# Kernel optimization log

Measured on AMD Instinct MI355X. Metric: run time of the kernel, lower is better.

Reference implementation:

```python
import jax, jax.numpy as jnp
import numpy as np

B, T, N, H, E, LH, OUT, D = 64, 12, 325, 64, 32, 128, 12, 1
META_OFF = 65  # x[..., :1] is the signal, x[..., 65:] is the 32-dim temporal meta input


def _mlp(meta, W1, b1, W2, b2):
    # meta: (B,E); W1: (4,E,LH); W2: (4,LH,O) -> (4,B,O); 4 = gates g,i,f,o
    h = jax.nn.relu(jnp.einsum('be,geh->gbh', meta, W1) + b1[:, None, :])
    return jnp.einsum('gbh,gho->gbo', h, W2) + b2[:, None, :]


def setup_inputs() -> dict:
    key = jax.random.key(0)
    ks = jax.random.split(key, 16)
    s = lambda k, shape: jax.random.normal(k, shape, dtype=jnp.float32) * 0.05
    return {
        'x': jax.random.normal(ks[0], (B, T, N, 1 + 64 + E), dtype=jnp.float32),
        'lwx_W1': s(ks[1], (4, E, LH)), 'lwx_b1': s(ks[2], (4, LH)),
        'lwx_W2': s(ks[3], (4, LH, D * H)), 'lwx_b2': s(ks[4], (4, D * H)),
        'lwh_W1': s(ks[5], (4, E, LH)), 'lwh_b1': s(ks[6], (4, LH)),
        'lwh_W2': s(ks[7], (4, LH, H * H)), 'lwh_b2': s(ks[8], (4, H * H)),
        'lb_W1': s(ks[9], (4, E, LH)), 'lb_b1': s(ks[10], (4, LH)),
        'lb_W2': s(ks[11], (4, LH, H)), 'lb_b2': s(ks[12], (4, H)),
        'fc1_W': s(ks[13], (H, H // 2)), 'fc1_b': jnp.zeros((H // 2,), jnp.float32),
        'fc2_W': s(ks[14], (H // 2, OUT * D)), 'fc2_b': jnp.zeros((OUT * D,), jnp.float32),
    }


def reference(x, lwx_W1, lwx_b1, lwx_W2, lwx_b2,
              lwh_W1, lwh_b1, lwh_W2, lwh_b2,
              lb_W1, lb_b1, lb_W2, lb_b2,
              fc1_W, fc1_b, fc2_W, fc2_b):
    batch = x.shape[0]
    meta = jnp.mean(x[:, :, 0, META_OFF:], axis=1)  # (B,E)
    xs = jnp.transpose(x[..., :D], (1, 0, 2, 3))    # (T,B,N,D)

    Wx = _mlp(meta, lwx_W1, lwx_b1, lwx_W2, lwx_b2).reshape(4, batch, D, H)
    Wh = _mlp(meta, lwh_W1, lwh_b1, lwh_W2, lwh_b2).reshape(4, batch, H, H)
    b = _mlp(meta, lb_W1, lb_b1, lb_W2, lb_b2).reshape(4, batch, 1, H)

    def step(carry, xt):
        h, c = carry
        # (4,B,N,H): per-batch weights -> batched matmuls for all 4 gates
        z = (jnp.einsum('bnd,gbdh->gbnh', xt, Wx)
             + jnp.einsum('bnh,gbhk->gbnk', h, Wh) + b)
        g = jnp.tanh(z[0])
        i = jax.nn.sigmoid(z[1])
        f = jax.nn.sigmoid(z[2])
        o = jax.nn.sigmoid(z[3])
        c = g * i + c * f
        h = jnp.tanh(c) * o
        return (h, c), None

    # h0=c0=0 reproduces the torch t==0 special case exactly
    h0 = jnp.zeros((batch, N, H), x.dtype)
    (h, _), _ = jax.lax.scan(step, (h0, h0), xs)

    out = jax.nn.relu(h)
    out = jax.nn.relu(out @ fc1_W + fc1_b) @ fc2_W + fc2_b  # (B,N,OUT*D)
    out = out.reshape(batch, N, OUT, D)
    return jnp.transpose(out, (0, 2, 1, 3))  # (B,OUT,N,D)
```

## Files before the change

kernel.cpp:

```cpp
#include <hip/hip_runtime.h>
#include <stdint.h>

#define TT 12
#define NN 325
#define HH 64
#define EE 32
#define LHH 128
#define OO 12
#define CIN 97
#define MOFF 65
#define BB 64

typedef __attribute__((ext_vector_type(8))) short bf8;
typedef __attribute__((ext_vector_type(4))) float f4;
typedef __attribute__((ext_vector_type(2))) float f2;

__device__ __forceinline__ float sigf(float x) {
  return __builtin_amdgcn_rcpf(1.f + __builtin_amdgcn_exp2f(-1.4426950408889634f * x));
}
__device__ __forceinline__ float tanhfast(float x) {
  return 1.f - 2.f * __builtin_amdgcn_rcpf(1.f + __builtin_amdgcn_exp2f(2.8853900817779268f * x));
}
__device__ __forceinline__ unsigned short f2bf(float f) {
  unsigned int u = __float_as_uint(f);
  u += 0x7fffu + ((u >> 16) & 1u);
  return (unsigned short)(u >> 16);
}
__device__ __forceinline__ float bf2f(unsigned short s) {
  return __uint_as_float(((unsigned int)s) << 16);
}

__global__ __launch_bounds__(256) void k_prep(
    const float* __restrict__ x,
    const float* __restrict__ xw1, const float* __restrict__ xb1,
    const float* __restrict__ xw2, const float* __restrict__ xb2,
    const float* __restrict__ hw1, const float* __restrict__ hb1,
    const float* __restrict__ hw2, const float* __restrict__ hb2,
    const float* __restrict__ bw1, const float* __restrict__ bb1,
    const float* __restrict__ bw2, const float* __restrict__ bb2,
    unsigned short* __restrict__ whb,
    float* __restrict__ wx_ws, float* __restrict__ bg_ws)
{
  const int bi = blockIdx.x, tid = threadIdx.x;
  const bool gemm = (bi < 1024);
  const int g  = gemm ? (bi >> 8) : ((bi - 1024) >> 2);
  const int bq = gemm ? (bi & 3) : ((bi - 1024) & 3);

  __shared__ float meta_s[16][EE];
  __shared__ float hbuf[2][16][132];

  for (int p = tid; p < 512; p += 256) {
    const int bl = p >> 5, e = p & 31;
    const int b = bq * 16 + bl;
    float s = 0.f;
    #pragma unroll
    for (int t = 0; t < TT; ++t)
      s += x[(size_t)((b * TT + t) * NN) * CIN + MOFF + e];
    meta_s[bl][e] = s * (1.f / 12.f);
  }
  __syncthreads();

  if (gemm) {
    const int i = (bi >> 2) & 63;
    for (int m = tid; m < 16 * LHH; m += 256) {
      const int bl = m >> 7, l = m & 127;
      float a = hb1[g * LHH + l];
      const float* w = hw1 + (size_t)g * (EE * LHH) + l;
      #pragma unroll
      for (int e = 0; e < EE; ++e) a = fmaf(meta_s[bl][e], w[e * LHH], a);
      hbuf[0][bl][l] = fmaxf(a, 0.f);
    }
    __syncthreads();

    const int r0 = (tid >> 5) * 2, j0 = (tid & 31) * 2;
    const float* w2p = hw2 + (size_t)(g * LHH) * 4096 + i * 64 + j0;
    float acc[2][2] = {};
    for (int l = 0; l < LHH; l += 4) {
      const f4 h0 = *(const f4*)&hbuf[0][r0][l];
      const f4 h1 = *(const f4*)&hbuf[0][r0 + 1][l];
      #pragma unroll
      for (int ll = 0; ll < 4; ++ll) {
        const f2 wv = *(const f2*)(w2p + (size_t)(l + ll) * 4096);
        acc[0][0] = fmaf(h0[ll], wv[0], acc[0][0]);
        acc[0][1] = fmaf(h0[ll], wv[1], acc[0][1]);
        acc[1][0] = fmaf(h1[ll], wv[0], acc[1][0]);
        acc[1][1] = fmaf(h1[ll], wv[1], acc[1][1]);
      }
    }

    const int kh = i >> 5, quad = (i >> 3) & 3, j8 = i & 7;
    #pragma unroll
    for (int rr = 0; rr < 2; ++rr) {
      const int b = bq * 16 + r0 + rr;
      #pragma unroll
      for (int jj = 0; jj < 2; ++jj) {
        const int j = j0 + jj;
        const float v = acc[rr][jj] + hb2[g * 4096 + i * 64 + j];
        const int col = g * 64 + j;
        const int nt = col >> 4, c16 = col & 15;
        const int lane = quad * 16 + c16;
        whb[(size_t)((b * 32 + kh * 16 + nt) * 64 + lane) * 8 + j8] = f2bf(v);
      }
    }
  } else {
    for (int m = tid; m < 2 * 16 * LHH; m += 256) {
      const int mlp = m >> 11, rem = m & 2047, bl = rem >> 7, l = rem & 127;
      const float* W1 = mlp ? bw1 : xw1;
      const float* B1 = mlp ? bb1 : xb1;
      float a = B1[g * LHH + l];
      const float* w = W1 + (size_t)g * (EE * LHH) + l;
      #pragma unroll
      for (int e = 0; e < EE; ++e) a = fmaf(meta_s[bl][e], w[e * LHH], a);
      hbuf[mlp][bl][l] = fmaxf(a, 0.f);
    }
    __syncthreads();

    const int h = tid & 63, bl0 = (tid >> 6) * 4;
    const float* wxp = xw2 + (size_t)g * (LHH * HH) + h;
    const float* wbp = bw2 + (size_t)g * (LHH * HH) + h;
    float accx[4], accb[4];
    #pragma unroll
    for (int k = 0; k < 4; ++k) {
      accx[k] = xb2[g * HH + h];
      accb[k] = bb2[g * HH + h];
    }
    for (int l = 0; l < LHH; ++l) {
      const float wxl = wxp[l * HH], wbl = wbp[l * HH];
      #pragma unroll
      for (int k = 0; k < 4; ++k) {
        accx[k] = fmaf(hbuf[0][bl0 + k][l], wxl, accx[k]);
        accb[k] = fmaf(hbuf[1][bl0 + k][l], wbl, accb[k]);
      }
    }
    #pragma unroll
    for (int k = 0; k < 4; ++k) {
      const int b = bq * 16 + bl0 + k;
      wx_ws[b * 256 + g * 64 + h] = accx[k];
      bg_ws[b * 256 + g * 64 + h] = accb[k];
    }
  }
}

__global__ __launch_bounds__(256, 3) void k_lstm(
    const float* __restrict__ x, const float* __restrict__ wx_ws,
    const float* __restrict__ bg_ws, const unsigned short* __restrict__ whb,
    const float* __restrict__ fc1W, const float* __restrict__ fc1b,
    const float* __restrict__ fc2W, const float* __restrict__ fc2b,
    float* __restrict__ out)
{
  const int rb = blockIdx.x, b = blockIdx.y, tid = threadIdx.x;
  const int wave = tid >> 6, lane = tid & 63, quad = lane >> 4, c16 = lane & 15;
  const int n0 = rb * 32;

  __shared__ __align__(16) unsigned short Hs[2][2][16][72];
  __shared__ float Xs[TT][32];
  __shared__ float fc1s[HH * 32];
  __shared__ float fc2s[32 * OO];
  __shared__ float HIDs[32][36];
  __shared__ float fc1bs[32];
  __shared__ float fc2bs[OO];

  for (int idx = tid; idx < TT * 32; idx += 256) {
    const int t = idx >> 5, r = idx & 31, n = n0 + r;
    Xs[t][r] = (n < NN) ? x[(size_t)((b * TT + t) * NN + n) * CIN] : 0.f;
  }
  for (int idx = tid; idx < HH * 32; idx += 256) fc1s[idx] = fc1W[idx];
  for (int idx = tid; idx < 32 * OO; idx += 256) fc2s[idx] = fc2W[idx];
  if (tid < 32) fc1bs[tid] = fc1b[tid];
  if (tid < OO) fc2bs[tid] = fc2b[tid];

  float wxv[4], bgv[4];
  #pragma unroll
  for (int g = 0; g < 4; ++g) {
    wxv[g] = wx_ws[b * 256 + g * 64 + wave * 16 + c16];
    bgv[g] = bg_ws[b * 256 + g * 64 + wave * 16 + c16];
  }
  bf8 wf[2][4];
  #pragma unroll
  for (int kh = 0; kh < 2; ++kh)
    #pragma unroll
    for (int g = 0; g < 4; ++g)
      wf[kh][g] = *(const bf8*)(whb + (size_t)((b * 32 + kh * 16 + g * 4 + wave) * 64 + lane) * 8);

  float cst[2][4];
  #pragma unroll
  for (int ta = 0; ta < 2; ++ta)
    #pragma unroll
    for (int r = 0; r < 4; ++r) cst[ta][r] = 0.f;

  __syncthreads();

  #pragma unroll 1
  for (int t = 0; t < TT; ++t) {
    bf8 af[2][2];
    if (t > 0) {
      #pragma unroll
      for (int ta = 0; ta < 2; ++ta) {
        af[ta][0] = *(const bf8*)&Hs[(t - 1) & 1][ta][c16][quad * 8];
        af[ta][1] = *(const bf8*)&Hs[(t - 1) & 1][ta][c16][32 + quad * 8];
      }
    }
    f4 ac[2][4];
    #pragma unroll
    for (int ta = 0; ta < 2; ++ta) {
      float xr[4];
      #pragma unroll
      for (int r = 0; r < 4; ++r) xr[r] = Xs[t][ta * 16 + quad * 4 + r];
      #pragma unroll
      for (int g = 0; g < 4; ++g)
        #pragma unroll
        for (int r = 0; r < 4; ++r)
          ac[ta][g][r] = fmaf(xr[r], wxv[g], bgv[g]);
    }
    if (t > 0) {
      #pragma unroll
      for (int ta = 0; ta < 2; ++ta)
        #pragma unroll
        for (int g = 0; g < 4; ++g) {
          ac[ta][g] = __builtin_amdgcn_mfma_f32_16x16x32_bf16(af[ta][0], wf[0][g], ac[ta][g], 0, 0, 0);
          ac[ta][g] = __builtin_amdgcn_mfma_f32_16x16x32_bf16(af[ta][1], wf[1][g], ac[ta][g], 0, 0, 0);
        }
    }
    #pragma unroll
    for (int ta = 0; ta < 2; ++ta)
      #pragma unroll
      for (int r = 0; r < 4; ++r) {
        const float gg = tanhfast(ac[ta][0][r]);
        const float ii = sigf(ac[ta][1][r]);
        const float ff = sigf(ac[ta][2][r]);
        const float oo = sigf(ac[ta][3][r]);
        const float cc = fmaf(gg, ii, cst[ta][r] * ff);
        cst[ta][r] = cc;
        const float hh = tanhfast(cc) * oo;
        Hs[t & 1][ta][quad * 4 + r][wave * 16 + c16] = f2bf(hh);
      }
    __syncthreads();
  }

  {
    const int row32 = tid & 31, uu = tid >> 5;
    const int ta = row32 >> 4, row = row32 & 15;
    float hacc[4];
    #pragma unroll
    for (int j = 0; j < 4; ++j) hacc[j] = fc1bs[uu * 4 + j];
    #pragma unroll
    for (int kc = 0; kc < 8; ++kc) {
      const bf8 hv = *(const bf8*)&Hs[1][ta][row][kc * 8];
      #pragma unroll
      for (int j8 = 0; j8 < 8; ++j8) {
        const float hk = fmaxf(bf2f((unsigned short)hv[j8]), 0.f);
        const int k = kc * 8 + j8;
        #pragma unroll
        for (int j = 0; j < 4; ++j)
          hacc[j] = fmaf(hk, fc1s[k * 32 + uu * 4 + j], hacc[j]);
      }
    }
    #pragma unroll
    for (int j = 0; j < 4; ++j)
      HIDs[row32][uu * 4 + j] = fmaxf(hacc[j], 0.f);
  }
  __syncthreads();
  for (int idx = tid; idx < 32 * OO; idx += 256) {
    const int o = idx >> 5, row32 = idx & 31;
    float a = fc2bs[o];
    #pragma unroll
    for (int k = 0; k < 32; ++k)
      a = fmaf(HIDs[row32][k], fc2s[k * OO + o], a);
    const int n = n0 + row32;
    if (n < NN)
      out[b * (OO * NN) + o * NN + n] = a;
  }
}

extern "C" void kernel_launch(void* const* d_in, const int* in_sizes, int n_in,
                              void* d_out, int out_size, void* d_ws, size_t ws_size,
                              hipStream_t stream) {
  const float* x    = (const float*)d_in[0];
  const float* xw1  = (const float*)d_in[1];
  const float* xb1  = (const float*)d_in[2];
  const float* xw2  = (const float*)d_in[3];
  const float* xb2  = (const float*)d_in[4];
  const float* hw1  = (const float*)d_in[5];
  const float* hb1  = (const float*)d_in[6];
  const float* hw2  = (const float*)d_in[7];
  const float* hb2  = (const float*)d_in[8];
  const float* bw1  = (const float*)d_in[9];
  const float* bb1  = (const float*)d_in[10];
  const float* bw2  = (const float*)d_in[11];
  const float* bb2  = (const float*)d_in[12];
  const float* fc1W = (const float*)d_in[13];
  const float* fc1b = (const float*)d_in[14];
  const float* fc2W = (const float*)d_in[15];
  const float* fc2b = (const float*)d_in[16];
  float* out = (float*)d_out;

  float* ws = (float*)d_ws;
  float* wx_ws = ws;
  float* bg_ws = ws + 16384;
  unsigned short* whb = (unsigned short*)(ws + 32768);

  k_prep<<<1040, 256, 0, stream>>>(x, xw1, xb1, xw2, xb2, hw1, hb1, hw2, hb2,
                                   bw1, bb1, bw2, bb2, whb, wx_ws, bg_ws);
  k_lstm<<<dim3(11, 64), 256, 0, stream>>>(x, wx_ws, bg_ws, whb,
                                           fc1W, fc1b, fc2W, fc2b, out);
}
```

Measured before the change: 236.7 us.

## Split meta mean into own kernel, stage W2 in LDS, pre-gather signal

Computes the temporal meta mean once per batch in a new small kernel, so the 1040 prep blocks no longer each re-read strided x. In the main prep kernel, the hw2 weight tile is first loaded cooperatively into shared memory in two halves, with coalesced reads, and the GEMM then reads from there. The gemm blocks also gather the signal channel of x into a compact buffer, so the LSTM kernel reads contiguous data instead of a stride of 97 floats. This adds one kernel launch and extra barriers, and raises the shared-memory footprint under a launch bound of 4 blocks.

Measured after the change: 232.1 us. -2.0%, faster.

```diff
diff --git a/kernel.cpp b/kernel.cpp
--- a/kernel.cpp
+++ b/kernel.cpp
@@ -30,15 +30,33 @@
   return __uint_as_float(((unsigned int)s) << 16);
 }
 
-__global__ __launch_bounds__(256) void k_prep(
-    const float* __restrict__ x,
+__global__ __launch_bounds__(256) void k_meta0(
+    const float* __restrict__ x, float* __restrict__ meta_ws)
+{
+  const int b = blockIdx.x, tid = threadIdx.x;
+  __shared__ float mpart[TT][EE];
+  for (int idx = tid; idx < TT * EE; idx += 256) {
+    const int t = idx >> 5, e = idx & 31;
+    mpart[t][e] = x[(size_t)((b * TT + t) * NN) * CIN + MOFF + e];
+  }
+  __syncthreads();
+  if (tid < EE) {
+    float s = 0.f;
+    #pragma unroll
+    for (int t = 0; t < TT; ++t) s += mpart[t][tid];
+    meta_ws[b * EE + tid] = s * (1.f / 12.f);
+  }
+}
+
+__global__ __launch_bounds__(256, 4) void k_main(
+    const float* __restrict__ x, const float* __restrict__ meta_ws,
     const float* __restrict__ xw1, const float* __restrict__ xb1,
     const float* __restrict__ xw2, const float* __restrict__ xb2,
     const float* __restrict__ hw1, const float* __restrict__ hb1,
     const float* __restrict__ hw2, const float* __restrict__ hb2,
     const float* __restrict__ bw1, const float* __restrict__ bb1,
     const float* __restrict__ bw2, const float* __restrict__ bb2,
-    unsigned short* __restrict__ whb,
+    unsigned short* __restrict__ whb, float* __restrict__ xg,
     float* __restrict__ wx_ws, float* __restrict__ bg_ws)
 {
   const int bi = blockIdx.x, tid = threadIdx.x;
@@ -48,20 +66,26 @@
 
   __shared__ float meta_s[16][EE];
   __shared__ float hbuf[2][16][132];
-
-  for (int p = tid; p < 512; p += 256) {
-    const int bl = p >> 5, e = p & 31;
-    const int b = bq * 16 + bl;
-    float s = 0.f;
-    #pragma unroll
-    for (int t = 0; t < TT; ++t)
-      s += x[(size_t)((b * TT + t) * NN) * CIN + MOFF + e];
-    meta_s[bl][e] = s * (1.f / 12.f);
-  }
+  __shared__ float w2s[64][64];
+
+  for (int p = tid; p < 16 * EE; p += 256)
+    meta_s[p >> 5][p & 31] = meta_ws[(bq * 16 + (p >> 5)) * EE + (p & 31)];
   __syncthreads();
 
   if (gemm) {
     const int i = (bi >> 2) & 63;
+
+    {
+      const int flat = bi * 244 + tid;
+      if (tid < 244 && flat < BB * TT * NN) {
+        const int b = flat / (TT * NN);
+        const int r = flat - b * (TT * NN);
+        const int t = r / NN;
+        const int n = r - t * NN;
+        xg[flat] = x[(size_t)((b * TT + t) * NN + n) * CIN];
+      }
+    }
+
     for (int m = tid; m < 16 * LHH; m += 256) {
       const int bl = m >> 7, l = m & 127;
       float a = hb1[g * LHH + l];
@@ -70,21 +94,27 @@
       for (int e = 0; e < EE; ++e) a = fmaf(meta_s[bl][e], w[e * LHH], a);
       hbuf[0][bl][l] = fmaxf(a, 0.f);
     }
-    __syncthreads();
 
     const int r0 = (tid >> 5) * 2, j0 = (tid & 31) * 2;
-    const float* w2p = hw2 + (size_t)(g * LHH) * 4096 + i * 64 + j0;
     float acc[2][2] = {};
-    for (int l = 0; l < LHH; l += 4) {
-      const f4 h0 = *(const f4*)&hbuf[0][r0][l];
-      const f4 h1 = *(const f4*)&hbuf[0][r0 + 1][l];
-      #pragma unroll
-      for (int ll = 0; ll < 4; ++ll) {
-        const f2 wv = *(const f2*)(w2p + (size_t)(l + ll) * 4096);
-        acc[0][0] = fmaf(h0[ll], wv[0], acc[0][0]);
-        acc[0][1] = fmaf(h0[ll], wv[1], acc[0][1]);
-        acc[1][0] = fmaf(h1[ll], wv[0], acc[1][0]);
-        acc[1][1] = fmaf(h1[ll], wv[1], acc[1][1]);
+    #pragma unroll
+    for (int half = 0; half < 2; ++half) {
+      __syncthreads();
+      for (int idx = tid; idx < 64 * 64; idx += 256)
+        w2s[idx >> 6][idx & 63] =
+            hw2[(size_t)(g * LHH + half * 64 + (idx >> 6)) * 4096 + i * 64 + (idx & 63)];
+      __syncthreads();
+      for (int l = 0; l < 64; l += 4) {
+        const f4 h0 = *(const f4*)&hbuf[0][r0][half * 64 + l];
+        const f4 h1 = *(const f4*)&hbuf[0][r0 + 1][half * 64 + l];
+        #pragma unroll
+        for (int ll = 0; ll < 4; ++ll) {
+          const f2 wv = *(const f2*)&w2s[l + ll][j0];
+          acc[0][0] = fmaf(h0[ll], wv[0], acc[0][0]);
+          acc[0][1] = fmaf(h0[ll], wv[1], acc[0][1]);
+          acc[1][0] = fmaf(h1[ll], wv[0], acc[1][0]);
+          acc[1][1] = fmaf(h1[ll], wv[1], acc[1][1]);
+        }
       }
     }
 
@@ -142,7 +172,7 @@
 }
 
 __global__ __launch_bounds__(256, 3) void k_lstm(
-    const float* __restrict__ x, const float* __restrict__ wx_ws,
+    const float* __restrict__ xg, const float* __restrict__ wx_ws,
     const float* __restrict__ bg_ws, const unsigned short* __restrict__ whb,
     const float* __restrict__ fc1W, const float* __restrict__ fc1b,
     const float* __restrict__ fc2W, const float* __restrict__ fc2b,
@@ -162,7 +192,7 @@
 
   for (int idx = tid; idx < TT * 32; idx += 256) {
     const int t = idx >> 5, r = idx & 31, n = n0 + r;
-    Xs[t][r] = (n < NN) ? x[(size_t)((b * TT + t) * NN + n) * CIN] : 0.f;
+    Xs[t][r] = (n < NN) ? xg[b * (TT * NN) + t * NN + n] : 0.f;
   }
   for (int idx = tid; idx < HH * 32; idx += 256) fc1s[idx] = fc1W[idx];
   for (int idx = tid; idx < 32 * OO; idx += 256) fc2s[idx] = fc2W[idx];
@@ -295,12 +325,16 @@
   float* out = (float*)d_out;
 
   float* ws = (float*)d_ws;
-  float* wx_ws = ws;
-  float* bg_ws = ws + 16384;
-  unsigned short* whb = (unsigned short*)(ws + 32768);
-
-  k_prep<<<1040, 256, 0, stream>>>(x, xw1, xb1, xw2, xb2, hw1, hb1, hw2, hb2,
-                                   bw1, bb1, bw2, bb2, whb, wx_ws, bg_ws);
-  k_lstm<<<dim3(11, 64), 256, 0, stream>>>(x, wx_ws, bg_ws, whb,
+  float* meta_ws = ws;
+  float* wx_ws   = ws + 2048;
+  float* bg_ws   = ws + 18432;
+  float* xg_ws   = ws + 34816;
+  unsigned short* whb = (unsigned short*)(ws + 34816 + BB * TT * NN);
+
+  k_meta0<<<64, 256, 0, stream>>>(x, meta_ws);
+  k_main<<<1040, 256, 0, stream>>>(x, meta_ws, xw1, xb1, xw2, xb2, hw1, hb1,
+                                   hw2, hb2, bw1, bb1, bw2, bb2, whb, xg_ws,
+                                   wx_ws, bg_ws);
+  k_lstm<<<dim3(11, 64), 256, 0, stream>>>(xg_ws, wx_ws, bg_ws, whb,
                                            fc1W, fc1b, fc2W, fc2b, out);
 }
```
